# Performance work log

Hardware: AMD Instinct MI355X
Metric: run time of the kernel (lower is better)

Reference implementation:

```python
import jax, jax.numpy as jnp
import numpy as np

N, D, O = 8000, 9, 1  # mulElements hard-codes 8000 rows; fc: 9 -> 1


def setup_inputs() -> dict:
    key = jax.random.key(0)
    ks = jax.random.split(key, 5)
    # scale x small so the (buggy) cumulative product over 8000 rows stays finite/nonzero
    x = jax.random.normal(ks[0], (N, D), dtype=jnp.float32) * 1e-3
    a1 = jnp.array([1.0], dtype=jnp.float32)
    c1 = jnp.array([0.0], dtype=jnp.float32)
    a2 = jnp.array([1.1], dtype=jnp.float32)
    c2 = jnp.array([5e-4], dtype=jnp.float32)
    w_fc1 = jax.random.normal(ks[1], (O, D), dtype=jnp.float32) / np.sqrt(D)
    b_fc1 = jax.random.normal(ks[2], (O,), dtype=jnp.float32) * 0.01
    w_fc2 = jax.random.normal(ks[3], (O, D), dtype=jnp.float32) / np.sqrt(D)
    b_fc2 = jax.random.normal(ks[4], (O,), dtype=jnp.float32) * 0.01
    return {"x": x, "a1": a1, "c1": c1, "a2": a2, "c2": c2,
            "w_fc1": w_fc1, "b_fc1": b_fc1, "w_fc2": w_fc2, "b_fc2": b_fc2}


def reference(x, a1, c1, a2, c2, w_fc1, b_fc1, w_fc2, b_fc2):
    # Gaussian memberships, [N, D]
    miu1 = jnp.exp(-(((x - c1) / a1) ** 2))
    miu2 = jnp.exp(-(((x - c2) / a2) ** 2))
    # mulElements: w_temp is NOT reset per row in the original code, so
    # w[i] = prod over rows 0..i of the row-product -> cumprod of row products.
    w1 = jnp.cumprod(jnp.prod(miu1, axis=1))  # [N]
    w2 = jnp.cumprod(jnp.prod(miu2, axis=1))  # [N]
    s = w1 + w2
    w1_bar = w1 / s  # [N]
    w2_bar = w2 / s  # [N]
    f1 = x @ w_fc1.T + b_fc1  # [N, 1]
    f2 = x @ w_fc2.T + b_fc2  # [N, 1]
    # torch broadcasting: [N] * [N,1] -> [N,N]
    out = f1 * w1_bar[None, :] + f2 * w2_bar[None, :]  # [N, N]
    return out
```

## Files before the change

### kernel.cpp

```cpp
#include <hip/hip_runtime.h>

#define NROWS 8000
#define DDIM 9
#define NCOL4 (NROWS / 4)
#define ROWS_PER_BLK 50
#define SCAN_T 1024
#define RPT 8

typedef float f32x4 __attribute__((ext_vector_type(4)));

__global__ __launch_bounds__(SCAN_T)
void anfis_prep(const float* __restrict__ x,
                const float* __restrict__ a1p, const float* __restrict__ c1p,
                const float* __restrict__ a2p, const float* __restrict__ c2p,
                const float* __restrict__ w_fc1, const float* __restrict__ b_fc1,
                const float* __restrict__ w_fc2, const float* __restrict__ b_fc2,
                float* __restrict__ w1bo, float* __restrict__ w2bo,
                float2* __restrict__ f12o) {
    __shared__ float sh1[SCAN_T];
    __shared__ float sh2[SCAN_T];
    const int t = threadIdx.x;
    const int r0 = t * RPT;

    const float inv_a1 = 1.0f / a1p[0];
    const float c1 = c1p[0];
    const float inv_a2 = 1.0f / a2p[0];
    const float c2 = c2p[0];
    const float bb1 = b_fc1[0];
    const float bb2 = b_fc2[0];
    float wf1[DDIM], wf2[DDIM];
#pragma unroll
    for (int j = 0; j < DDIM; ++j) { wf1[j] = w_fc1[j]; wf2[j] = w_fc2[j]; }

    float cs1[RPT], cs2[RPT];
    float run1 = 0.f, run2 = 0.f;
#pragma unroll
    for (int k = 0; k < RPT; ++k) {
        int r = r0 + k;
        float s1 = 0.f, s2 = 0.f, d1 = 0.f, d2 = 0.f;
        if (r < NROWS) {
#pragma unroll
            for (int j = 0; j < DDIM; ++j) {
                float xv = x[r * DDIM + j];
                float t1 = (xv - c1) * inv_a1;
                float t2 = (xv - c2) * inv_a2;
                s1 += t1 * t1;
                s2 += t2 * t2;
                d1 += xv * wf1[j];
                d2 += xv * wf2[j];
            }
            f12o[r] = make_float2(d1 + bb1, d2 + bb2);
        }
        run1 += s1;
        run2 += s2;
        cs1[k] = run1;
        cs2[k] = run2;
    }
    sh1[t] = run1;
    sh2[t] = run2;
    __syncthreads();
    for (int off = 1; off < SCAN_T; off <<= 1) {
        float v1 = 0.f, v2 = 0.f;
        if (t >= off) { v1 = sh1[t - off]; v2 = sh2[t - off]; }
        __syncthreads();
        sh1[t] += v1;
        sh2[t] += v2;
        __syncthreads();
    }
    const float pre1 = (t > 0) ? sh1[t - 1] : 0.f;
    const float pre2 = (t > 0) ? sh2[t - 1] : 0.f;
#pragma unroll
    for (int k = 0; k < RPT; ++k) {
        int r = r0 + k;
        if (r < NROWS) {
            float a = pre1 + cs1[k];
            float b = pre2 + cs2[k];
            float e = expf(a - b);
            float inv = 1.0f / (1.0f + e);
            w1bo[r] = inv;
            w2bo[r] = e * inv;
        }
    }
}

__global__ __launch_bounds__(256)
void anfis_out(const float2* __restrict__ f12,
               const float* __restrict__ w1b, const float* __restrict__ w2b,
               float* __restrict__ out) {
    const int j4 = blockIdx.x * 256 + threadIdx.x;
    if (j4 >= NCOL4) return;
    const int i0 = blockIdx.y * ROWS_PER_BLK;

    const f32x4 u = ((const f32x4*)w1b)[j4];
    const f32x4 v = ((const f32x4*)w2b)[j4];
    f32x4* orow = (f32x4*)out + (size_t)i0 * NCOL4 + j4;

#pragma unroll 2
    for (int k = 0; k < ROWS_PER_BLK; ++k) {
        const float2 ab = f12[i0 + k];
        f32x4 o = ab.x * u + ab.y * v;
        __builtin_nontemporal_store(o, orow);
        orow += NCOL4;
    }
}

extern "C" void kernel_launch(void* const* d_in, const int* in_sizes, int n_in,
                              void* d_out, int out_size, void* d_ws, size_t ws_size,
                              hipStream_t stream) {
    const float* x     = (const float*)d_in[0];
    const float* a1    = (const float*)d_in[1];
    const float* c1    = (const float*)d_in[2];
    const float* a2    = (const float*)d_in[3];
    const float* c2    = (const float*)d_in[4];
    const float* w_fc1 = (const float*)d_in[5];
    const float* b_fc1 = (const float*)d_in[6];
    const float* w_fc2 = (const float*)d_in[7];
    const float* b_fc2 = (const float*)d_in[8];
    float* out = (float*)d_out;

    float* ws   = (float*)d_ws;
    float* w1b  = ws;
    float* w2b  = ws + 8000;
    float2* f12 = (float2*)(ws + 16000);

    anfis_prep<<<1, SCAN_T, 0, stream>>>(x, a1, c1, a2, c2,
                                         w_fc1, b_fc1, w_fc2, b_fc2,
                                         w1b, w2b, f12);
    anfis_out<<<dim3((NCOL4 + 255) / 256, NROWS / ROWS_PER_BLK), 256, 0, stream>>>(
        f12, w1b, w2b, out);
}
```

Baseline: 306.4 us.

## Split single-block scan into parallel wave scans plus chunk-prefix kernel

The single 1024-thread prep block becomes three stages. A multi-block row kernel computes per-row sums and does 64-lane shuffle inclusive scans per wave. A tiny kernel scans the 125 wave totals. The output kernel now adds the chunk prefix and computes the exp/normalise weights inline, so the serial one-block prep stage is spread across the GPU. The cost is an extra kernel launch and redundant exp work in every output block row group (160 times per column).

```diff
diff --git a/kernel.cpp b/kernel.cpp
--- a/kernel.cpp
+++ b/kernel.cpp
@@ -4,62 +4,63 @@
 #define DDIM 9
 #define NCOL4 (NROWS / 4)
 #define ROWS_PER_BLK 50
-#define SCAN_T 1024
-#define RPT 8
+#define NCHUNK 125
 
 typedef float f32x4 __attribute__((ext_vector_type(4)));
 
-__global__ __launch_bounds__(SCAN_T)
-void anfis_prep(const float* __restrict__ x,
+__global__ __launch_bounds__(256)
+void anfis_rows(const float* __restrict__ x,
                 const float* __restrict__ a1p, const float* __restrict__ c1p,
                 const float* __restrict__ a2p, const float* __restrict__ c2p,
                 const float* __restrict__ w_fc1, const float* __restrict__ b_fc1,
                 const float* __restrict__ w_fc2, const float* __restrict__ b_fc2,
-                float* __restrict__ w1bo, float* __restrict__ w2bo,
-                float2* __restrict__ f12o) {
-    __shared__ float sh1[SCAN_T];
-    __shared__ float sh2[SCAN_T];
-    const int t = threadIdx.x;
-    const int r0 = t * RPT;
+                float* __restrict__ cs1o, float* __restrict__ cs2o,
+                float2* __restrict__ f12o,
+                float* __restrict__ t1o, float* __restrict__ t2o) {
+    const int wid  = (blockIdx.x * 256 + threadIdx.x) >> 6;
+    const int lane = threadIdx.x & 63;
+    if (wid >= NCHUNK) return;
+    const int r = wid * 64 + lane;
 
     const float inv_a1 = 1.0f / a1p[0];
     const float c1 = c1p[0];
     const float inv_a2 = 1.0f / a2p[0];
     const float c2 = c2p[0];
-    const float bb1 = b_fc1[0];
-    const float bb2 = b_fc2[0];
-    float wf1[DDIM], wf2[DDIM];
+
+    float s1 = 0.f, s2 = 0.f, d1 = 0.f, d2 = 0.f;
 #pragma unroll
-    for (int j = 0; j < DDIM; ++j) { wf1[j] = w_fc1[j]; wf2[j] = w_fc2[j]; }
+    for (int j = 0; j < DDIM; ++j) {
+        float xv = x[r * DDIM + j];
+        float u1 = (xv - c1) * inv_a1;
+        float u2 = (xv - c2) * inv_a2;
+        s1 += u1 * u1;
+        s2 += u2 * u2;
+        d1 += xv * w_fc1[j];
+        d2 += xv * w_fc2[j];
+    }
+    f12o[r] = make_float2(d1 + b_fc1[0], d2 + b_fc2[0]);
 
-    float cs1[RPT], cs2[RPT];
-    float run1 = 0.f, run2 = 0.f;
 #pragma unroll
-    for (int k = 0; k < RPT; ++k) {
-        int r = r0 + k;
-        float s1 = 0.f, s2 = 0.f, d1 = 0.f, d2 = 0.f;
-        if (r < NROWS) {
-#pragma unroll
-            for (int j = 0; j < DDIM; ++j) {
-                float xv = x[r * DDIM + j];
-                float t1 = (xv - c1) * inv_a1;
-                float t2 = (xv - c2) * inv_a2;
-                s1 += t1 * t1;
-                s2 += t2 * t2;
-                d1 += xv * wf1[j];
-                d2 += xv * wf2[j];
-            }
-            f12o[r] = make_float2(d1 + bb1, d2 + bb2);
-        }
-        run1 += s1;
-        run2 += s2;
-        cs1[k] = run1;
-        cs2[k] = run2;
+    for (int d = 1; d < 64; d <<= 1) {
+        float n1 = __shfl_up(s1, d, 64);
+        float n2 = __shfl_up(s2, d, 64);
+        if (lane >= d) { s1 += n1; s2 += n2; }
     }
-    sh1[t] = run1;
-    sh2[t] = run2;
+    cs1o[r] = s1;
+    cs2o[r] = s2;
+    if (lane == 63) { t1o[wid] = s1; t2o[wid] = s2; }
+}
+
+__global__ __launch_bounds__(128)
+void anfis_chunkscan(const float* __restrict__ t1, const float* __restrict__ t2,
+                     float* __restrict__ p1, float* __restrict__ p2) {
+    __shared__ float sh1[128];
+    __shared__ float sh2[128];
+    const int t = threadIdx.x;
+    sh1[t] = (t < NCHUNK) ? t1[t] : 0.f;
+    sh2[t] = (t < NCHUNK) ? t2[t] : 0.f;
     __syncthreads();
-    for (int off = 1; off < SCAN_T; off <<= 1) {
+    for (int off = 1; off < 128; off <<= 1) {
         float v1 = 0.f, v2 = 0.f;
         if (t >= off) { v1 = sh1[t - off]; v2 = sh2[t - off]; }
         __syncthreads();
@@ -67,34 +68,34 @@
         sh2[t] += v2;
         __syncthreads();
     }
-    const float pre1 = (t > 0) ? sh1[t - 1] : 0.f;
-    const float pre2 = (t > 0) ? sh2[t - 1] : 0.f;
-#pragma unroll
-    for (int k = 0; k < RPT; ++k) {
-        int r = r0 + k;
-        if (r < NROWS) {
-            float a = pre1 + cs1[k];
-            float b = pre2 + cs2[k];
-            float e = expf(a - b);
-            float inv = 1.0f / (1.0f + e);
-            w1bo[r] = inv;
-            w2bo[r] = e * inv;
-        }
+    if (t < NCHUNK) {
+        p1[t] = (t > 0) ? sh1[t - 1] : 0.f;
+        p2[t] = (t > 0) ? sh2[t - 1] : 0.f;
     }
 }
 
 __global__ __launch_bounds__(256)
 void anfis_out(const float2* __restrict__ f12,
-               const float* __restrict__ w1b, const float* __restrict__ w2b,
+               const float* __restrict__ cs1, const float* __restrict__ cs2,
+               const float* __restrict__ p1, const float* __restrict__ p2,
                float* __restrict__ out) {
     const int j4 = blockIdx.x * 256 + threadIdx.x;
     if (j4 >= NCOL4) return;
+    const int c = j4 >> 4;
+
+    f32x4 a = ((const f32x4*)cs1)[j4] + p1[c];
+    f32x4 b = ((const f32x4*)cs2)[j4] + p2[c];
+    f32x4 u, v;
+#pragma unroll
+    for (int q = 0; q < 4; ++q) {
+        float e = expf(a[q] - b[q]);
+        float inv = 1.0f / (1.0f + e);
+        u[q] = inv;
+        v[q] = e * inv;
+    }
+
     const int i0 = blockIdx.y * ROWS_PER_BLK;
-
-    const f32x4 u = ((const f32x4*)w1b)[j4];
-    const f32x4 v = ((const f32x4*)w2b)[j4];
     f32x4* orow = (f32x4*)out + (size_t)i0 * NCOL4 + j4;
-
 #pragma unroll 2
     for (int k = 0; k < ROWS_PER_BLK; ++k) {
         const float2 ab = f12[i0 + k];
@@ -119,13 +120,17 @@
     float* out = (float*)d_out;
 
     float* ws   = (float*)d_ws;
-    float* w1b  = ws;
-    float* w2b  = ws + 8000;
+    float* cs1  = ws;
+    float* cs2  = ws + 8000;
     float2* f12 = (float2*)(ws + 16000);
+    float* t1   = ws + 32000;
+    float* t2   = ws + 32125;
+    float* p1   = ws + 32250;
+    float* p2   = ws + 32375;
 
-    anfis_prep<<<1, SCAN_T, 0, stream>>>(x, a1, c1, a2, c2,
-                                         w_fc1, b_fc1, w_fc2, b_fc2,
-                                         w1b, w2b, f12);
+    anfis_rows<<<(NCHUNK * 64 + 255) / 256, 256, 0, stream>>>(
+        x, a1, c1, a2, c2, w_fc1, b_fc1, w_fc2, b_fc2, cs1, cs2, f12, t1, t2);
+    anfis_chunkscan<<<1, 128, 0, stream>>>(t1, t2, p1, p2);
     anfis_out<<<dim3((NCOL4 + 255) / 256, NROWS / ROWS_PER_BLK), 256, 0, stream>>>(
-        f12, w1b, w2b, out);
+        f12, cs1, cs2, p1, p2, out);
 }
```

Result: faster. 274.9 us (-10.3%).
